# Kernel optimization log

Measured on AMD Instinct MI355X. Metric: run time of the kernel, lower is better.

The kernel has to match this reference:

```python
import jax, jax.numpy as jnp
import numpy as np


def _bilinear_ac(img, H, W):
    """Bilinear resize with align_corners=True. img: [B, C, h, w] -> [B, C, H, W]."""
    B, C, h, w = img.shape
    ys = jnp.linspace(0.0, h - 1.0, H)
    xs = jnp.linspace(0.0, w - 1.0, W)
    y0 = jnp.floor(ys).astype(jnp.int32)
    x0 = jnp.floor(xs).astype(jnp.int32)
    y1 = jnp.minimum(y0 + 1, h - 1)
    x1 = jnp.minimum(x0 + 1, w - 1)
    wy = (ys - y0).astype(img.dtype)  # [H]
    wx = (xs - x0).astype(img.dtype)  # [W]
    top = img[:, :, y0, :]            # [B, C, H, w]
    bot = img[:, :, y1, :]
    row = top * (1.0 - wy)[None, None, :, None] + bot * wy[None, None, :, None]
    left = row[:, :, :, x0]           # [B, C, H, W]
    right = row[:, :, :, x1]
    return left * (1.0 - wx)[None, None, None, :] + right * wx[None, None, None, :]


def setup_inputs() -> dict:
    key = jax.random.key(0)
    k1, k2, k3 = jax.random.split(key, 3)
    B, F, h, w = 16, 256, 64, 64
    H, W = 512, 512
    K = 21
    feature_map = jax.random.normal(k1, (B, F, h, w), dtype=jnp.float32)
    x = jax.random.uniform(k2, (B, 3, H, W), dtype=jnp.float32)
    conv_w = jax.random.normal(k3, (K, F), dtype=jnp.float32) * 0.05
    conv_b = jnp.zeros((K,), dtype=jnp.float32)
    return {"feature_map": feature_map, "x": x, "conv_w": conv_w, "conv_b": conv_b}


def reference(feature_map, x, conv_w, conv_b):
    B, _, H, W = x.shape
    # 1x1 conv: feature_dim -> num_classes
    logits = jnp.einsum('bfhw,kf->bkhw', feature_map, conv_w) + conv_b[None, :, None, None]
    seg = jax.nn.softmax(logits, axis=1)                 # [B, K, h, w]
    seg = _bilinear_ac(seg, H, W)                        # [B, K, H, W]
    xp = jnp.transpose(x, (0, 2, 3, 1))                  # [B, H, W, C]
    # per-class masked mean pooling (the python loop, fused into one einsum)
    q = jnp.einsum('bhwc,bkhw->bkc', xp, seg) / (H * W)  # [B, K, C]
    # broadcast dot-product attention maps
    attn = jnp.einsum('bhwc,bkc->bkhw', xp, q)           # [B, K, H, W]
    return attn
```

## Files before the change

kernel.cpp:

```cpp
#include <hip/hip_runtime.h>

#define BN 16
#define FD 256
#define SH 64
#define SW 64
#define BH 512
#define BW 512
#define KN 21
#define SP (SH*SW)
#define BP (BH*BW)

#define SEG_BLOCKS 64
#define DOWNX_BLOCKS (BN*3*BH*SW/256)

typedef float f32x4 __attribute__((ext_vector_type(4)));

__device__ __forceinline__ float adj_w(int big, int small) {
    double t = (double)big * (63.0 / 511.0);
    int i0 = (int)t;
    double fr = t - (double)i0;
    int i1 = i0 + 1; if (i1 > 63) i1 = 63;
    float w = 0.0f;
    if (i0 == small) w += (float)(1.0 - fr);
    if (i1 == small) w += (float)fr;
    return w;
}

__device__ __forceinline__ void adj_range(int small, int& lo, int& hi) {
    lo = (int)floorf((small - 1) * (511.0f / 63.0f)); if (lo < 0) lo = 0;
    hi = (int)ceilf((small + 1) * (511.0f / 63.0f));  if (hi > 511) hi = 511;
}

__device__ __forceinline__ void seg_body(int blk, int tid,
                                         const float* __restrict__ fm,
                                         const float* __restrict__ cw,
                                         const float* __restrict__ cb,
                                         float* __restrict__ seg) {
    int gid = blk * 256 + tid;
    int b   = gid >> 10;
    int p4  = gid & 1023;
    const f32x4* fmb = (const f32x4*)(fm + (size_t)b * FD * SP) + p4;

    f32x4 acc[KN];
#pragma unroll
    for (int k = 0; k < KN; ++k) acc[k] = (f32x4)0.0f;

#pragma unroll 2
    for (int f = 0; f < FD; ++f) {
        f32x4 v = fmb[f * (SP / 4)];
#pragma unroll
        for (int k = 0; k < KN; ++k)
            acc[k] += v * cw[k * FD + f];
    }

    f32x4 mx = (f32x4)(-1e30f);
#pragma unroll
    for (int k = 0; k < KN; ++k) {
        acc[k] += cb[k];
        mx.x = fmaxf(mx.x, acc[k].x); mx.y = fmaxf(mx.y, acc[k].y);
        mx.z = fmaxf(mx.z, acc[k].z); mx.w = fmaxf(mx.w, acc[k].w);
    }
    f32x4 s = (f32x4)0.0f;
#pragma unroll
    for (int k = 0; k < KN; ++k) {
        acc[k].x = expf(acc[k].x - mx.x); acc[k].y = expf(acc[k].y - mx.y);
        acc[k].z = expf(acc[k].z - mx.z); acc[k].w = expf(acc[k].w - mx.w);
        s += acc[k];
    }
    f32x4 inv;
    inv.x = 1.0f / s.x; inv.y = 1.0f / s.y; inv.z = 1.0f / s.z; inv.w = 1.0f / s.w;

    f32x4* segb = (f32x4*)(seg + (size_t)b * KN * SP) + p4;
#pragma unroll
    for (int k = 0; k < KN; ++k) segb[k * (SP / 4)] = acc[k] * inv;
}

__device__ __forceinline__ void downx_body(int blk, int tid,
                                           const float* __restrict__ x,
                                           float* __restrict__ tmpA) {
    int gid = blk * 256 + tid;
    int s  = gid & 63;
    int Y  = (gid >> 6) & 511;
    int bc = gid >> 15;
    const float* row = x + ((size_t)bc * BH + Y) * BW;
    int lo, hi; adj_range(s, lo, hi);
    float acc = 0.0f;
    for (int X = lo; X <= hi; ++X) acc = fmaf(adj_w(X, s), row[X], acc);
    tmpA[gid] = acc;
}

__global__ __launch_bounds__(256) void k_phase1(const float* __restrict__ fm,
                                                const float* __restrict__ cw,
                                                const float* __restrict__ cb,
                                                const float* __restrict__ x,
                                                float* __restrict__ seg,
                                                float* __restrict__ tmpA) {
    if (blockIdx.x < SEG_BLOCKS) seg_body(blockIdx.x, threadIdx.x, fm, cw, cb, seg);
    else                         downx_body(blockIdx.x - SEG_BLOCKS, threadIdx.x, x, tmpA);
}

__global__ __launch_bounds__(256) void k_downy(const float* __restrict__ tmpA,
                                               float* __restrict__ xd) {
    int gid = blockIdx.x * 256 + threadIdx.x;
    int s  = gid & 63;
    int r  = (gid >> 6) & 63;
    int bc = gid >> 12;
    const float* base = tmpA + (size_t)bc * BH * SW + s;
    int lo, hi; adj_range(r, lo, hi);
    float acc = 0.0f;
    for (int Y = lo; Y <= hi; ++Y) acc = fmaf(adj_w(Y, r), base[(size_t)Y * SW], acc);
    xd[gid] = acc;
}

__global__ __launch_bounds__(256) void k_q(const float* __restrict__ seg,
                                           const float* __restrict__ xd,
                                           float* __restrict__ q) {
    int b = blockIdx.x / KN, k = blockIdx.x % KN;
    const float* sg = seg + ((size_t)b * KN + k) * SP;
    const float* xb = xd + (size_t)b * 3 * SP;
    float a0 = 0.f, a1 = 0.f, a2 = 0.f;
    for (int p = threadIdx.x; p < SP; p += 256) {
        float sv = sg[p];
        a0 = fmaf(sv, xb[p], a0);
        a1 = fmaf(sv, xb[SP + p], a1);
        a2 = fmaf(sv, xb[2 * SP + p], a2);
    }
    __shared__ float red[3][256];
    red[0][threadIdx.x] = a0; red[1][threadIdx.x] = a1; red[2][threadIdx.x] = a2;
    __syncthreads();
    for (int off = 128; off > 0; off >>= 1) {
        if (threadIdx.x < (unsigned)off) {
            red[0][threadIdx.x] += red[0][threadIdx.x + off];
            red[1][threadIdx.x] += red[1][threadIdx.x + off];
            red[2][threadIdx.x] += red[2][threadIdx.x + off];
        }
        __syncthreads();
    }
    if (threadIdx.x == 0) {
        const float scale = 1.0f / (float)BP;
        float* qo = q + ((size_t)b * KN + k) * 3;
        qo[0] = red[0][0] * scale;
        qo[1] = red[1][0] * scale;
        qo[2] = red[2][0] * scale;
    }
}

__global__ __launch_bounds__(256) void k_attn(const float* __restrict__ x,
                                              const float* __restrict__ q,
                                              float* __restrict__ out) {
    int b   = blockIdx.x >> 8;
    int blk = blockIdx.x & 255;
    int p4  = blk * 256 + threadIdx.x;

    const f32x4* xb = (const f32x4*)(x + (size_t)b * 3 * BP);
    f32x4 x0 = xb[p4];
    f32x4 x1 = xb[BP / 4 + p4];
    f32x4 x2 = xb[2 * (BP / 4) + p4];

    __shared__ float qs[KN * 3];
    if (threadIdx.x < KN * 3) qs[threadIdx.x] = q[(size_t)b * KN * 3 + threadIdx.x];
    __syncthreads();

    f32x4* ob = (f32x4*)(out + (size_t)b * KN * BP) + p4;
#pragma unroll
    for (int k = 0; k < KN; ++k) {
        float q0 = qs[k * 3], q1 = qs[k * 3 + 1], q2 = qs[k * 3 + 2];
        f32x4 r = x0 * q0 + x1 * q1 + x2 * q2;
        __builtin_nontemporal_store(r, ob + (size_t)k * (BP / 4));
    }
}

extern "C" void kernel_launch(void* const* d_in, const int* in_sizes, int n_in,
                              void* d_out, int out_size, void* d_ws, size_t ws_size,
                              hipStream_t stream) {
    const float* fm = (const float*)d_in[0];
    const float* x  = (const float*)d_in[1];
    const float* cw = (const float*)d_in[2];
    const float* cb = (const float*)d_in[3];
    float* out = (float*)d_out;

    float* seg  = (float*)d_ws;
    float* tmpA = seg  + (size_t)BN * KN * SP;
    float* xd   = tmpA + (size_t)BN * 3 * BH * SW;
    float* q    = xd   + (size_t)BN * 3 * SP;

    k_phase1<<<SEG_BLOCKS + DOWNX_BLOCKS, 256, 0, stream>>>(fm, cw, cb, x, seg, tmpA);
    k_downy <<<BN * 3 * SP / 256,         256, 0, stream>>>(tmpA, xd);
    k_q     <<<BN * KN,                   256, 0, stream>>>(seg, xd, q);
    k_attn  <<<BN * (BP / 1024),          256, 0, stream>>>(x, q, out);
}
```

Before: 509.4 us.

## Spread seg conv over more blocks and split q reduction with atomics

The softmax-conv body now gives each thread one spatial pixel instead of four, so it runs on four times as many blocks and holds fewer accumulators per thread. The q reduction is split into four partial blocks per (batch, class). Each block reduces with wave shuffles and adds its partial sum into q with atomics, and k_downy zeroes q first. The goal is more parallelism in the small, latency-bound stages, at the cost of scalar loads in the conv and a nondeterministic order of the atomic sums.

Measured after the change: 480.0 us. -5.8%, faster.

```diff
diff --git a/kernel.cpp b/kernel.cpp
--- a/kernel.cpp
+++ b/kernel.cpp
@@ -10,8 +10,9 @@
 #define SP (SH*SW)
 #define BP (BH*BW)
 
-#define SEG_BLOCKS 64
+#define SEG_BLOCKS 256
 #define DOWNX_BLOCKS (BN*3*BH*SW/256)
+#define QSPLIT 4
 
 typedef float f32x4 __attribute__((ext_vector_type(4)));
 
@@ -37,42 +38,33 @@
                                          const float* __restrict__ cb,
                                          float* __restrict__ seg) {
     int gid = blk * 256 + tid;
-    int b   = gid >> 10;
-    int p4  = gid & 1023;
-    const f32x4* fmb = (const f32x4*)(fm + (size_t)b * FD * SP) + p4;
+    int b   = gid >> 12;
+    int p   = gid & 4095;
+    const float* fmb = fm + (size_t)b * FD * SP + p;
 
-    f32x4 acc[KN];
+    float acc[KN];
 #pragma unroll
-    for (int k = 0; k < KN; ++k) acc[k] = (f32x4)0.0f;
+    for (int k = 0; k < KN; ++k) acc[k] = 0.0f;
 
-#pragma unroll 2
+#pragma unroll 4
     for (int f = 0; f < FD; ++f) {
-        f32x4 v = fmb[f * (SP / 4)];
+        float v = fmb[(size_t)f * SP];
 #pragma unroll
         for (int k = 0; k < KN; ++k)
-            acc[k] += v * cw[k * FD + f];
+            acc[k] = fmaf(v, cw[k * FD + f], acc[k]);
     }
 
-    f32x4 mx = (f32x4)(-1e30f);
+    float mx = -1e30f;
 #pragma unroll
-    for (int k = 0; k < KN; ++k) {
-        acc[k] += cb[k];
-        mx.x = fmaxf(mx.x, acc[k].x); mx.y = fmaxf(mx.y, acc[k].y);
-        mx.z = fmaxf(mx.z, acc[k].z); mx.w = fmaxf(mx.w, acc[k].w);
-    }
-    f32x4 s = (f32x4)0.0f;
+    for (int k = 0; k < KN; ++k) { acc[k] += cb[k]; mx = fmaxf(mx, acc[k]); }
+    float s = 0.0f;
 #pragma unroll
-    for (int k = 0; k < KN; ++k) {
-        acc[k].x = expf(acc[k].x - mx.x); acc[k].y = expf(acc[k].y - mx.y);
-        acc[k].z = expf(acc[k].z - mx.z); acc[k].w = expf(acc[k].w - mx.w);
-        s += acc[k];
-    }
-    f32x4 inv;
-    inv.x = 1.0f / s.x; inv.y = 1.0f / s.y; inv.z = 1.0f / s.z; inv.w = 1.0f / s.w;
+    for (int k = 0; k < KN; ++k) { acc[k] = expf(acc[k] - mx); s += acc[k]; }
+    float inv = 1.0f / s;
 
-    f32x4* segb = (f32x4*)(seg + (size_t)b * KN * SP) + p4;
+    float* segb = seg + (size_t)b * KN * SP + p;
 #pragma unroll
-    for (int k = 0; k < KN; ++k) segb[k * (SP / 4)] = acc[k] * inv;
+    for (int k = 0; k < KN; ++k) segb[(size_t)k * SP] = acc[k] * inv;
 }
 
 __device__ __forceinline__ void downx_body(int blk, int tid,
@@ -100,7 +92,12 @@
 }
 
 __global__ __launch_bounds__(256) void k_downy(const float* __restrict__ tmpA,
-                                               float* __restrict__ xd) {
+                                               float* __restrict__ xd,
+                                               float* __restrict__ q) {
+    if (blockIdx.x < 4) {
+        int i = blockIdx.x * 256 + threadIdx.x;
+        if (i < BN * KN * 3) q[i] = 0.0f;
+    }
     int gid = blockIdx.x * 256 + threadIdx.x;
     int s  = gid & 63;
     int r  = (gid >> 6) & 63;
@@ -115,33 +112,37 @@
 __global__ __launch_bounds__(256) void k_q(const float* __restrict__ seg,
                                            const float* __restrict__ xd,
                                            float* __restrict__ q) {
-    int b = blockIdx.x / KN, k = blockIdx.x % KN;
+    int bk   = blockIdx.x / QSPLIT;
+    int part = blockIdx.x % QSPLIT;
+    int b = bk / KN, k = bk % KN;
     const float* sg = seg + ((size_t)b * KN + k) * SP;
     const float* xb = xd + (size_t)b * 3 * SP;
     float a0 = 0.f, a1 = 0.f, a2 = 0.f;
-    for (int p = threadIdx.x; p < SP; p += 256) {
+    int p0 = part * (SP / QSPLIT);
+    for (int p = p0 + threadIdx.x; p < p0 + SP / QSPLIT; p += 256) {
         float sv = sg[p];
         a0 = fmaf(sv, xb[p], a0);
         a1 = fmaf(sv, xb[SP + p], a1);
         a2 = fmaf(sv, xb[2 * SP + p], a2);
     }
-    __shared__ float red[3][256];
-    red[0][threadIdx.x] = a0; red[1][threadIdx.x] = a1; red[2][threadIdx.x] = a2;
+    for (int off = 32; off > 0; off >>= 1) {
+        a0 += __shfl_down(a0, off, 64);
+        a1 += __shfl_down(a1, off, 64);
+        a2 += __shfl_down(a2, off, 64);
+    }
+    __shared__ float red[4][3];
+    int lane = threadIdx.x & 63, w = threadIdx.x >> 6;
+    if (lane == 0) { red[w][0] = a0; red[w][1] = a1; red[w][2] = a2; }
     __syncthreads();
-    for (int off = 128; off > 0; off >>= 1) {
-        if (threadIdx.x < (unsigned)off) {
-            red[0][threadIdx.x] += red[0][threadIdx.x + off];
-            red[1][threadIdx.x] += red[1][threadIdx.x + off];
-            red[2][threadIdx.x] += red[2][threadIdx.x + off];
-        }
-        __syncthreads();
-    }
     if (threadIdx.x == 0) {
         const float scale = 1.0f / (float)BP;
+        float s0 = red[0][0] + red[1][0] + red[2][0] + red[3][0];
+        float s1 = red[0][1] + red[1][1] + red[2][1] + red[3][1];
+        float s2 = red[0][2] + red[1][2] + red[2][2] + red[3][2];
         float* qo = q + ((size_t)b * KN + k) * 3;
-        qo[0] = red[0][0] * scale;
-        qo[1] = red[1][0] * scale;
-        qo[2] = red[2][0] * scale;
+        atomicAdd(qo + 0, s0 * scale);
+        atomicAdd(qo + 1, s1 * scale);
+        atomicAdd(qo + 2, s2 * scale);
     }
 }
 
@@ -185,7 +186,7 @@
     float* q    = xd   + (size_t)BN * 3 * SP;
 
     k_phase1<<<SEG_BLOCKS + DOWNX_BLOCKS, 256, 0, stream>>>(fm, cw, cb, x, seg, tmpA);
-    k_downy <<<BN * 3 * SP / 256,         256, 0, stream>>>(tmpA, xd);
-    k_q     <<<BN * KN,                   256, 0, stream>>>(seg, xd, q);
+    k_downy <<<BN * 3 * SP / 256,         256, 0, stream>>>(tmpA, xd, q);
+    k_q     <<<BN * KN * QSPLIT,          256, 0, stream>>>(seg, xd, q);
     k_attn  <<<BN * (BP / 1024),          256, 0, stream>>>(x, q, out);
 }
```
